# Performance work log

Hardware: AMD Instinct MI355X
Metric: run time of the kernel (lower is better)

Reference implementation:

```python
import jax, jax.numpy as jnp
import numpy as np

T, B, IN, H, H2 = 32, 65536, 27, 10, 5


def setup_inputs() -> dict:
    key = jax.random.key(0)
    ks = jax.random.split(key, 9)
    s = lambda k, shape, fan: jax.random.normal(k, shape, jnp.float32) / np.sqrt(fan)
    return {
        "word": jax.random.normal(ks[0], (T, B, IN), jnp.float32),
        "W_ih": s(ks[1], (4 * H, IN), IN),
        "W_hh": s(ks[2], (4 * H, H), H),
        "b_ih": s(ks[3], (4 * H,), H),
        "b_hh": s(ks[4], (4 * H,), H),
        "W_fc": s(ks[5], (H2, H), H),
        "b_fc": s(ks[6], (H2,), H),
        "W_out": s(ks[7], (1, H2), H2),
        "b_out": s(ks[8], (1,), H2),
    }


def reference(word, W_ih, W_hh, b_ih, b_hh, W_fc, b_fc, W_out, b_out):
    """Batched LSTMCell recurrence over characters with ReLU on both h and c
    (as in the original forward_one_letter; dropout is identity in eval mode),
    then FC(10->5) -> ReLU -> Linear(5->1) -> sigmoid on the final hidden."""
    Bsz = word.shape[1]
    h0 = jnp.zeros((Bsz, H), word.dtype)
    c0 = jnp.zeros((Bsz, H), word.dtype)

    def step(carry, x):  # x: [B, IN]
        h, c = carry
        gates = x @ W_ih.T + b_ih + h @ W_hh.T + b_hh  # [B, 4H]
        i, f, g, o = jnp.split(gates, 4, axis=-1)      # torch gate order i,f,g,o
        i = jax.nn.sigmoid(i)
        f = jax.nn.sigmoid(f)
        g = jnp.tanh(g)
        o = jax.nn.sigmoid(o)
        c_new = f * c + i * g
        h_new = o * jnp.tanh(c_new)
        # original applies ReLU to both carried hidden and cell states
        return (jax.nn.relu(h_new), jax.nn.relu(c_new)), None

    (h, c), _ = jax.lax.scan(step, (h0, c0), word)
    y = jax.nn.relu(h @ W_fc.T + b_fc)   # [B, 5]
    y = y @ W_out.T + b_out              # [B, 1]
    return jax.nn.sigmoid(y)
```

## Files before the change

### kernel.cpp

```cpp
#include <hip/hip_runtime.h>

#define T_STEPS 32
#define BATCH   65536
#define IN_DIM  27
#define H_DIM   10
#define H2_DIM  5

typedef _Float16 f16_t;
typedef _Float16 f16x4 __attribute__((ext_vector_type(4)));
typedef float    f32x4 __attribute__((ext_vector_type(4)));

__device__ __forceinline__ float fast_exp2(float v) { return __builtin_amdgcn_exp2f(v); }
__device__ __forceinline__ float fast_rcp(float v)  { return __builtin_amdgcn_rcpf(v); }
__device__ __forceinline__ float fast_sigmoid(float v) {
    return fast_rcp(1.f + fast_exp2(v * -1.4426950408889634f));
}
__device__ __forceinline__ float fast_tanh(float v) {
    return 1.f - 2.f * fast_rcp(1.f + fast_exp2(v * 2.8853900817779268f));
}

__device__ __forceinline__ f32x4 load4u(const float* p) {
    f32x4 v; __builtin_memcpy(&v, p, 16); return v;
}

__global__
__attribute__((amdgpu_flat_work_group_size(256, 256), amdgpu_waves_per_eu(4, 4)))
void lstm_fused_mfma(
    const float* __restrict__ word,
    const float* __restrict__ W_ih,
    const float* __restrict__ W_hh,
    const float* __restrict__ b_ih,
    const float* __restrict__ b_hh,
    const float* __restrict__ W_fc,
    const float* __restrict__ b_fc,
    const float* __restrict__ W_out,
    const float* __restrict__ b_out,
    float* __restrict__ out)
{
    __shared__ __align__(16) f16_t s_h[4][16 * 20];

    const int tid  = threadIdx.x;
    const int lane = tid & 63;
    const int w    = tid >> 6;
    const int bn   = lane & 15;
    const int kg   = lane >> 4;
    const int e0   = blockIdx.x * 64 + w * 16;

    const bool gok = (bn < H_DIM);
    f16x4 bfx0[4], bfx1[4], bfh[4];
    float bias[4];
#pragma unroll
    for (int nt = 0; nt < 4; ++nt) {
        const int g = nt * H_DIM + bn;
        bias[nt] = gok ? (b_ih[g] + b_hh[g]) : 0.f;
#pragma unroll
        for (int i = 0; i < 4; ++i) {
            const int k = kg * 4 + i;
            bfx0[nt][i] = (f16_t)(gok ? W_ih[g * IN_DIM + k] : 0.f);
            bfx1[nt][i] = (f16_t)((gok && k >= 5) ? W_ih[g * IN_DIM + 11 + k] : 0.f);
            bfh[nt][i]  = (f16_t)((gok && k < H_DIM) ? W_hh[g * H_DIM + k] : 0.f);
        }
    }

    f16_t* tb = &s_h[w][0];
    {
        f16x4 z = {(f16_t)0.f, (f16_t)0.f, (f16_t)0.f, (f16_t)0.f};
        *(f16x4*)(tb + bn * 20 + kg * 4) = z;
    }

    float c[4];
#pragma unroll
    for (int r = 0; r < 4; ++r) c[r] = 0.f;

    const float* xbase = word + (size_t)(e0 + bn) * IN_DIM;
    const size_t tstep = (size_t)BATCH * IN_DIM;
    const int c0 = kg * 4, c1 = 11 + kg * 4;

    f32x4 xa = load4u(xbase + c0);
    f32x4 xb = load4u(xbase + c1);

    for (int t = 0; t < T_STEPS; ++t) {
        const float* xr = xbase + (size_t)((t + 1 < T_STEPS) ? t + 1 : t) * tstep;
        f32x4 na = load4u(xr + c0);
        f32x4 nb = load4u(xr + c1);

        const f16x4 ah = *(const f16x4*)(tb + bn * 20 + kg * 4);

        f16x4 ax0, ax1;
#pragma unroll
        for (int i = 0; i < 4; ++i) { ax0[i] = (f16_t)xa[i]; ax1[i] = (f16_t)xb[i]; }

        f32x4 acc[4];
#pragma unroll
        for (int nt = 0; nt < 4; ++nt) {
            f32x4 a = {bias[nt], bias[nt], bias[nt], bias[nt]};
            a = __builtin_amdgcn_mfma_f32_16x16x16f16(ax0, bfx0[nt], a, 0, 0, 0);
            a = __builtin_amdgcn_mfma_f32_16x16x16f16(ax1, bfx1[nt], a, 0, 0, 0);
            a = __builtin_amdgcn_mfma_f32_16x16x16f16(ah,  bfh[nt],  a, 0, 0, 0);
            acc[nt] = a;
        }

#pragma unroll
        for (int reg = 0; reg < 4; ++reg) {
            const float iv = fast_sigmoid(acc[0][reg]);
            const float fv = fast_sigmoid(acc[1][reg]);
            const float gv = fast_tanh   (acc[2][reg]);
            const float ov = fast_sigmoid(acc[3][reg]);
            const float cn = fmaf(fv, c[reg], iv * gv);
            c[reg] = fmaxf(cn, 0.f);
            const float hv = ov * fast_tanh(c[reg]);
            tb[(kg * 4 + reg) * 20 + bn] = (f16_t)hv;
        }

        xa = na; xb = nb;
    }

    if (lane < 16) {
        float hv[H_DIM];
#pragma unroll
        for (int u = 0; u < H_DIM; ++u) hv[u] = (float)tb[lane * 20 + u];
        float accv = b_out[0];
#pragma unroll
        for (int p = 0; p < H2_DIM; ++p) {
            float y = b_fc[p];
#pragma unroll
            for (int m = 0; m < H_DIM; ++m) y = fmaf(W_fc[p * H_DIM + m], hv[m], y);
            y = fmaxf(y, 0.f);
            accv = fmaf(W_out[p], y, accv);
        }
        out[e0 + lane] = fast_sigmoid(accv);
    }
}

extern "C" void kernel_launch(void* const* d_in, const int* in_sizes, int n_in,
                              void* d_out, int out_size, void* d_ws, size_t ws_size,
                              hipStream_t stream) {
    const float* word  = (const float*)d_in[0];
    const float* W_ih  = (const float*)d_in[1];
    const float* W_hh  = (const float*)d_in[2];
    const float* b_ih  = (const float*)d_in[3];
    const float* b_hh  = (const float*)d_in[4];
    const float* W_fc  = (const float*)d_in[5];
    const float* b_fc  = (const float*)d_in[6];
    const float* W_out = (const float*)d_in[7];
    const float* b_out = (const float*)d_in[8];
    float* out = (float*)d_out;

    lstm_fused_mfma<<<BATCH / 64, 256, 0, stream>>>(
        word, W_ih, W_hh, b_ih, b_hh, W_fc, b_fc, W_out, b_out, out);
}
```

Measured before the change: 54.91 us.

## Software-pipeline input projection MFMAs one step ahead of recurrence

Moves the x-dependent MFMA work (input projection plus bias) for step t+1 off the recurrent critical path by computing it while step t's h-dependent MFMA and gate math run, using double-buffered accumulators and a manual 2x unroll. Prefetch distance of global loads grows to three steps ahead, and f32-to-f16 conversion uses packed cvt_pkrtz. This costs extra registers for the buffered accumulators and prefetched inputs, which may matter under the fixed waves-per-eu bound. Round-toward-zero conversion slightly changes rounding versus the default cast.

Measured after the change: 57.50 us. +4.7%, slower.

```diff
diff --git a/kernel.cpp b/kernel.cpp
--- a/kernel.cpp
+++ b/kernel.cpp
@@ -8,6 +8,7 @@
 
 typedef _Float16 f16_t;
 typedef _Float16 f16x4 __attribute__((ext_vector_type(4)));
+typedef __fp16   h16x2 __attribute__((ext_vector_type(2)));
 typedef float    f32x4 __attribute__((ext_vector_type(4)));
 
 __device__ __forceinline__ float fast_exp2(float v) { return __builtin_amdgcn_exp2f(v); }
@@ -21,6 +22,13 @@
 
 __device__ __forceinline__ f32x4 load4u(const float* p) {
     f32x4 v; __builtin_memcpy(&v, p, 16); return v;
+}
+
+__device__ __forceinline__ f16x4 cvt4(f32x4 v) {
+    union { h16x2 h2[2]; f16x4 h4; } u;
+    u.h2[0] = __builtin_amdgcn_cvt_pkrtz(v[0], v[1]);
+    u.h2[1] = __builtin_amdgcn_cvt_pkrtz(v[2], v[3]);
+    return u.h4;
 }
 
 __global__
@@ -48,11 +56,12 @@
 
     const bool gok = (bn < H_DIM);
     f16x4 bfx0[4], bfx1[4], bfh[4];
-    float bias[4];
+    f32x4 biasv[4];
 #pragma unroll
     for (int nt = 0; nt < 4; ++nt) {
         const int g = nt * H_DIM + bn;
-        bias[nt] = gok ? (b_ih[g] + b_hh[g]) : 0.f;
+        const float bv = gok ? (b_ih[g] + b_hh[g]) : 0.f;
+        biasv[nt] = (f32x4){bv, bv, bv, bv};
 #pragma unroll
         for (int i = 0; i < 4; ++i) {
             const int k = kg * 4 + i;
@@ -76,44 +85,67 @@
     const size_t tstep = (size_t)BATCH * IN_DIM;
     const int c0 = kg * 4, c1 = 11 + kg * 4;
 
-    f32x4 xa = load4u(xbase + c0);
-    f32x4 xb = load4u(xbase + c1);
+    f32x4 xaccA[4], xaccB[4];
+    f32x4 xaC, xbC, xaN, xbN;
+    {
+        f32x4 x0a = load4u(xbase + c0);
+        f32x4 x0b = load4u(xbase + c1);
+        xaC = load4u(xbase + tstep + c0);
+        xbC = load4u(xbase + tstep + c1);
+        xaN = load4u(xbase + 2 * tstep + c0);
+        xbN = load4u(xbase + 2 * tstep + c1);
+        const f16x4 a0 = cvt4(x0a), a1 = cvt4(x0b);
+#pragma unroll
+        for (int nt = 0; nt < 4; ++nt)
+            xaccA[nt] = __builtin_amdgcn_mfma_f32_16x16x16f16(
+                a1, bfx1[nt],
+                __builtin_amdgcn_mfma_f32_16x16x16f16(a0, bfx0[nt], biasv[nt], 0, 0, 0),
+                0, 0, 0);
+    }
 
-    for (int t = 0; t < T_STEPS; ++t) {
-        const float* xr = xbase + (size_t)((t + 1 < T_STEPS) ? t + 1 : t) * tstep;
-        f32x4 na = load4u(xr + c0);
-        f32x4 nb = load4u(xr + c1);
+#define STEP_BODY(XC, XN, T)                                                     \
+    {                                                                            \
+                                      \
+        const int tn = ((T) + 3 < T_STEPS) ? (T) + 3 : (T_STEPS - 1);            \
+        const float* xr = xbase + (size_t)tn * tstep;                            \
+        f32x4 fa = load4u(xr + c0);                                              \
+        f32x4 fb = load4u(xr + c1);                                              \
+              \
+        const f16x4 a0 = cvt4(xaC), a1 = cvt4(xbC);                              \
+        _Pragma("unroll")                                                        \
+        for (int nt = 0; nt < 4; ++nt)                                           \
+            XN[nt] = __builtin_amdgcn_mfma_f32_16x16x16f16(                      \
+                a1, bfx1[nt],                                                    \
+                __builtin_amdgcn_mfma_f32_16x16x16f16(a0, bfx0[nt], biasv[nt],   \
+                                                      0, 0, 0), 0, 0, 0);        \
+             \
+        const f16x4 ah = *(const f16x4*)(tb + bn * 20 + kg * 4);                 \
+        f32x4 acc[4];                                                            \
+        _Pragma("unroll")                                                        \
+        for (int nt = 0; nt < 4; ++nt)                                           \
+            acc[nt] = __builtin_amdgcn_mfma_f32_16x16x16f16(ah, bfh[nt],         \
+                                                            XC[nt], 0, 0, 0);   \
+        _Pragma("unroll")                                                        \
+        for (int reg = 0; reg < 4; ++reg) {                                      \
+            const float iv = fast_sigmoid(acc[0][reg]);                          \
+            const float fv = fast_sigmoid(acc[1][reg]);                          \
+            const float gv = fast_tanh   (acc[2][reg]);                          \
+            const float ov = fast_sigmoid(acc[3][reg]);                          \
+            const float cn = fmaf(fv, c[reg], iv * gv);                          \
+            c[reg] = fmaxf(cn, 0.f);                                             \
+            const float hv = ov * fast_tanh(c[reg]);                             \
+            tb[(kg * 4 + reg) * 20 + bn] = (f16_t)hv;                            \
+        }                                                                        \
+                                                              \
+        xaC = xaN; xbC = xbN; xaN = fa; xbN = fb;                                \
+    }
 
-        const f16x4 ah = *(const f16x4*)(tb + bn * 20 + kg * 4);
-
-        f16x4 ax0, ax1;
-#pragma unroll
-        for (int i = 0; i < 4; ++i) { ax0[i] = (f16_t)xa[i]; ax1[i] = (f16_t)xb[i]; }
-
-        f32x4 acc[4];
-#pragma unroll
-        for (int nt = 0; nt < 4; ++nt) {
-            f32x4 a = {bias[nt], bias[nt], bias[nt], bias[nt]};
-            a = __builtin_amdgcn_mfma_f32_16x16x16f16(ax0, bfx0[nt], a, 0, 0, 0);
-            a = __builtin_amdgcn_mfma_f32_16x16x16f16(ax1, bfx1[nt], a, 0, 0, 0);
-            a = __builtin_amdgcn_mfma_f32_16x16x16f16(ah,  bfh[nt],  a, 0, 0, 0);
-            acc[nt] = a;
-        }
-
-#pragma unroll
-        for (int reg = 0; reg < 4; ++reg) {
-            const float iv = fast_sigmoid(acc[0][reg]);
-            const float fv = fast_sigmoid(acc[1][reg]);
-            const float gv = fast_tanh   (acc[2][reg]);
-            const float ov = fast_sigmoid(acc[3][reg]);
-            const float cn = fmaf(fv, c[reg], iv * gv);
-            c[reg] = fmaxf(cn, 0.f);
-            const float hv = ov * fast_tanh(c[reg]);
-            tb[(kg * 4 + reg) * 20 + bn] = (f16_t)hv;
-        }
-
-        xa = na; xb = nb;
+#pragma unroll 1
+    for (int t = 0; t < T_STEPS; t += 2) {
+        STEP_BODY(xaccA, xaccB, t)
+        STEP_BODY(xaccB, xaccA, t + 1)
     }
+#undef STEP_BODY
 
     if (lane < 16) {
         float hv[H_DIM];
```

## Stage input slabs through double-buffered shared memory with coalesced vector loads

Applied to the files above, without the earlier changes.

Each wave now loads its contiguous 16x27 input slab per timestep with coalesced aligned 16-byte loads, converts to fp16, and scatters it into a padded shared-memory tile. It double-buffers the tile and prefetches two steps ahead. Previously each lane issued overlapping unaligned 16-byte loads from strided rows. The MFMA operands are then read from LDS. This cuts redundant global traffic and unaligned accesses, at the cost of extra LDS stores and reads and some scattered 2-byte LDS writes, which may bank-conflict.

Result: slower. 61.99 us (+12.9%).

```diff
diff --git a/kernel.cpp b/kernel.cpp
--- a/kernel.cpp
+++ b/kernel.cpp
@@ -5,6 +5,7 @@
 #define IN_DIM  27
 #define H_DIM   10
 #define H2_DIM  5
+#define XROW    36
 
 typedef _Float16 f16_t;
 typedef _Float16 f16x4 __attribute__((ext_vector_type(4)));
@@ -17,10 +18,6 @@
 }
 __device__ __forceinline__ float fast_tanh(float v) {
     return 1.f - 2.f * fast_rcp(1.f + fast_exp2(v * 2.8853900817779268f));
-}
-
-__device__ __forceinline__ f32x4 load4u(const float* p) {
-    f32x4 v; __builtin_memcpy(&v, p, 16); return v;
 }
 
 __global__
@@ -37,6 +34,7 @@
     const float* __restrict__ b_out,
     float* __restrict__ out)
 {
+    __shared__ __align__(16) f16_t s_x[4][2][16 * XROW];
     __shared__ __align__(16) f16_t s_h[4][16 * 20];
 
     const int tid  = threadIdx.x;
@@ -55,40 +53,82 @@
         bias[nt] = gok ? (b_ih[g] + b_hh[g]) : 0.f;
 #pragma unroll
         for (int i = 0; i < 4; ++i) {
-            const int k = kg * 4 + i;
+            const int k  = kg * 4 + i;
+            const int k2 = 16 + kg * 4 + i;
             bfx0[nt][i] = (f16_t)(gok ? W_ih[g * IN_DIM + k] : 0.f);
-            bfx1[nt][i] = (f16_t)((gok && k >= 5) ? W_ih[g * IN_DIM + 11 + k] : 0.f);
+            bfx1[nt][i] = (f16_t)((gok && k2 < IN_DIM) ? W_ih[g * IN_DIM + k2] : 0.f);
             bfh[nt][i]  = (f16_t)((gok && k < H_DIM) ? W_hh[g * H_DIM + k] : 0.f);
         }
     }
 
-    f16_t* tb = &s_h[w][0];
+    f16_t* xb0 = &s_x[w][0][0];
+    f16_t* xb1 = &s_x[w][1][0];
+    f16_t* tb  = &s_h[w][0];
+
     {
         f16x4 z = {(f16_t)0.f, (f16_t)0.f, (f16_t)0.f, (f16_t)0.f};
+        f16_t* base = &s_x[w][0][0];
+        for (int s = lane; s < 2 * 16 * XROW / 4; s += 64)
+            *(f16x4*)(base + s * 4) = z;
         *(f16x4*)(tb + bn * 20 + kg * 4) = z;
+    }
+
+    int off1[4], off2[4];
+#pragma unroll
+    for (int j = 0; j < 4; ++j) {
+        const int g1 = 4 * lane + j;
+        off1[j] = (g1 / IN_DIM) * XROW + (g1 % IN_DIM);
+        const int g2 = 256 + 4 * lane + j;
+        off2[j] = (g2 / IN_DIM) * XROW + (g2 % IN_DIM);
+    }
+    const bool has2 = (lane < 44);
+
+    const size_t tstep = (size_t)BATCH * IN_DIM;
+    const float* slabbase = word + (size_t)e0 * IN_DIM;
+
+    {
+        f32x4 v1 = *(const f32x4*)(slabbase + 4 * lane);
+#pragma unroll
+        for (int j = 0; j < 4; ++j) xb0[off1[j]] = (f16_t)v1[j];
+        if (has2) {
+            f32x4 v2 = *(const f32x4*)(slabbase + 256 + 4 * lane);
+#pragma unroll
+            for (int j = 0; j < 4; ++j) xb0[off2[j]] = (f16_t)v2[j];
+        }
+    }
+    f32x4 p1, p2;
+    {
+        const float* slab1 = slabbase + tstep;
+        p1 = *(const f32x4*)(slab1 + 4 * lane);
+        p2 = has2 ? *(const f32x4*)(slab1 + 256 + 4 * lane) : (f32x4){0.f, 0.f, 0.f, 0.f};
     }
 
     float c[4];
 #pragma unroll
     for (int r = 0; r < 4; ++r) c[r] = 0.f;
 
-    const float* xbase = word + (size_t)(e0 + bn) * IN_DIM;
-    const size_t tstep = (size_t)BATCH * IN_DIM;
-    const int c0 = kg * 4, c1 = 11 + kg * 4;
+#pragma unroll 2
+    for (int t = 0; t < T_STEPS; ++t) {
+        f16_t* xcur = (t & 1) ? xb1 : xb0;
+        f16_t* xnxt = (t & 1) ? xb0 : xb1;
 
-    f32x4 xa = load4u(xbase + c0);
-    f32x4 xb = load4u(xbase + c1);
+        const f16x4 ax0 = *(const f16x4*)(xcur + bn * XROW + kg * 4);
+        const f16x4 ax1 = *(const f16x4*)(xcur + bn * XROW + 16 + kg * 4);
+        const f16x4 ah  = *(const f16x4*)(tb + bn * 20 + kg * 4);
 
-    for (int t = 0; t < T_STEPS; ++t) {
-        const float* xr = xbase + (size_t)((t + 1 < T_STEPS) ? t + 1 : t) * tstep;
-        f32x4 na = load4u(xr + c0);
-        f32x4 nb = load4u(xr + c1);
+#pragma unroll
+        for (int j = 0; j < 4; ++j) xnxt[off1[j]] = (f16_t)p1[j];
+        if (has2) {
+#pragma unroll
+            for (int j = 0; j < 4; ++j) xnxt[off2[j]] = (f16_t)p2[j];
+        }
 
-        const f16x4 ah = *(const f16x4*)(tb + bn * 20 + kg * 4);
-
-        f16x4 ax0, ax1;
-#pragma unroll
-        for (int i = 0; i < 4; ++i) { ax0[i] = (f16_t)xa[i]; ax1[i] = (f16_t)xb[i]; }
+        {
+            const int tn = (t + 2 < T_STEPS) ? t + 2 : (T_STEPS - 1);
+            const float* slab = slabbase + (size_t)tn * tstep;
+            p1 = *(const f32x4*)(slab + 4 * lane);
+            if (has2) p2 = *(const f32x4*)(slab + 256 + 4 * lane);
+        }
 
         f32x4 acc[4];
 #pragma unroll
@@ -111,8 +151,6 @@
             const float hv = ov * fast_tanh(c[reg]);
             tb[(kg * 4 + reg) * 20 + bn] = (f16_t)hv;
         }
-
-        xa = na; xb = nb;
     }
 
     if (lane < 16) {
```
